# Kernel tuning notes

Measured on AMD Instinct MI355X. Metric: run time of the kernel, lower is better.

The kernel has to match this reference:

```python
import jax, jax.numpy as jnp
import numpy as np

B, N, IN_F, OUT_F = 32, 1024, 256, 256


def setup_inputs() -> dict:
    key = jax.random.key(0)
    k_adj, k_feat, k_w, k_b = jax.random.split(key, 4)
    adjacency = jax.random.uniform(k_adj, (B, N, N), dtype=jnp.float32)  # [B,N,N]
    features = jax.random.normal(k_feat, (B, N, IN_F), dtype=jnp.float32)  # [B,N,in]
    # 'thomas' init ~ uniform(-1/sqrt(fan_in), 1/sqrt(fan_in)) style; scale is
    # irrelevant to correctness-checking, use scaled normal.
    weight = jax.random.normal(k_w, (IN_F, OUT_F), dtype=jnp.float32) / np.sqrt(IN_F)
    bias = jax.random.normal(k_b, (OUT_F,), dtype=jnp.float32) / np.sqrt(IN_F)
    return {"adjacency": adjacency, "features": features, "weight": weight, "bias": bias}


def reference(adjacency, features, weight, bias) -> jnp.ndarray:
    # support = features @ weight : [B,N,out]
    support = jnp.einsum("bni,io->bno", features, weight)
    # output = bmm(adjacency, support) : [B,N,out]
    output = jnp.einsum("bnm,bmo->bno", adjacency, support)
    return output + bias
```

## Files before the change

### kernel.cpp

```cpp
#include <hip/hip_runtime.h>
#include <hip/hip_bf16.h>


typedef __attribute__((__ext_vector_type__(4))) float  f32x4;
typedef __attribute__((__ext_vector_type__(8))) __bf16 bf16x8;
typedef __attribute__((__ext_vector_type__(4))) __bf16 bf16x4;

#define BK 64

__device__ __forceinline__ void gld16(const void* g, void* l) {
  __builtin_amdgcn_global_load_lds(
      (const __attribute__((address_space(1))) unsigned int*)g,
      (__attribute__((address_space(3))) unsigned int*)l, 16, 0, 0);
}

__global__ __launch_bounds__(256) void k_wt(const float* __restrict__ w,
                                            __bf16* __restrict__ Wt) {
  __shared__ __bf16 T[64][65];
  const int bi = blockIdx.x >> 2;
  const int bj = blockIdx.x & 3;
  const int t  = threadIdx.x;
  const int r  = t >> 2;
  const int q  = t & 3;
  const float* src = w + (size_t)(bi * 64 + r) * 256 + bj * 64 + q * 16;
#pragma unroll
  for (int u = 0; u < 4; ++u) {
    f32x4 v = *(const f32x4*)(src + u * 4);
    T[r][q * 16 + u * 4 + 0] = (__bf16)v[0];
    T[r][q * 16 + u * 4 + 1] = (__bf16)v[1];
    T[r][q * 16 + u * 4 + 2] = (__bf16)v[2];
    T[r][q * 16 + u * 4 + 3] = (__bf16)v[3];
  }
  __syncthreads();
  bf16x8 h0, h1;
#pragma unroll
  for (int u = 0; u < 8; ++u) {
    h0[u] = T[q * 16 + u][r];
    h1[u] = T[q * 16 + 8 + u][r];
  }
  __bf16* d0 = Wt + ((size_t)(bi * 8 + q * 2) * 256 + (bj * 64 + r)) * 8;
  *(bf16x8*)d0          = h0;
  *(bf16x8*)(d0 + 2048) = h1;
}

template <int KTOT, int LDA, bool EPI_ST>
__global__ __launch_bounds__(512, 2) void k_gemm(
    const float* __restrict__ Aall, const __bf16* __restrict__ Bg_all,
    const float* __restrict__ bias, float* __restrict__ Out,
    __bf16* __restrict__ St) {
  __shared__ __bf16 Af[2][128 * 64];
  __shared__ __bf16 Bf[2][8 * 256 * 8];

  const int tid  = threadIdx.x;
  const int lane = tid & 63;
  const int wid  = tid >> 6;
  const int wr   = wid >> 2;
  const int wc   = wid & 3;
  const int l16  = lane & 15;
  const int g    = lane >> 4;

  int b, mblk;
  const float*  Ablk;
  const __bf16* Bblk;
  if constexpr (EPI_ST) {
    const int bx = blockIdx.x;
    b    = bx >> 3;
    mblk = bx & 7;
    Ablk = Aall + (size_t)bx * 128 * LDA;
    Bblk = Bg_all;
  } else {
    const int h  = blockIdx.x;
    const int lg = (h & 7) * 32 + (h >> 3);
    b    = lg >> 3;
    mblk = lg & 7;
    Ablk = Aall + (size_t)b * 1024 * 1024 + (size_t)mblk * 128 * LDA;
    Bblk = Bg_all + (size_t)b * 262144;
  }

  const int    srow = tid >> 2;
  const int    sq   = tid & 3;
  const float* asrc = Ablk + (size_t)srow * LDA + sq * 16;
  const int wof0 = srow * 64 + (((sq * 2)     ^ (srow & 7)) << 3);
  const int wof1 = srow * 64 + (((sq * 2 + 1) ^ (srow & 7)) << 3);

  const __bf16* bS[4];
#pragma unroll
  for (int i = 0; i < 4; ++i) bS[i] = Bblk + (size_t)(i * 512 + tid) * 8;

#define LOADA(S, k0)                                                          \
  {                                                                           \
    _Pragma("unroll") for (int u = 0; u < 4; ++u)                             \
        S[u] = *(const f32x4*)(asrc + (k0) + u * 4);                          \
  }
#define ISSUEB(buf, k0)                                                       \
  {                                                                           \
    const size_t koff = (size_t)((k0) >> 3) * 2048;                           \
    _Pragma("unroll") for (int i = 0; i < 4; ++i)                             \
        gld16(bS[i] + koff, &Bf[buf][(i * 512 + wid * 64) * 8]);              \
  }
#define CVTW(S, buf)                                                          \
  {                                                                           \
    bf16x8 h0 = {(__bf16)S[0][0], (__bf16)S[0][1], (__bf16)S[0][2],           \
                 (__bf16)S[0][3], (__bf16)S[1][0], (__bf16)S[1][1],           \
                 (__bf16)S[1][2], (__bf16)S[1][3]};                           \
    bf16x8 h1 = {(__bf16)S[2][0], (__bf16)S[2][1], (__bf16)S[2][2],           \
                 (__bf16)S[2][3], (__bf16)S[3][0], (__bf16)S[3][1],           \
                 (__bf16)S[3][2], (__bf16)S[3][3]};                           \
    *(bf16x8*)&Af[buf][wof0] = h0;                                            \
    *(bf16x8*)&Af[buf][wof1] = h1;                                            \
  }

  f32x4 S0[4], S1[4];

  f32x4 acc[4][4];
#pragma unroll
  for (int m = 0; m < 4; ++m)
#pragma unroll
    for (int n = 0; n < 4; ++n) acc[m][n] = (f32x4){0.f, 0.f, 0.f, 0.f};

  auto compute = [&](int buf) {
#pragma unroll
    for (int ks = 0; ks < 2; ++ks) {
      bf16x8 af[4], bv[4];
#pragma unroll
      for (int m = 0; m < 4; ++m) {
        const int row  = wr * 64 + m * 16 + l16;
        const int slot = (ks * 4 + g) ^ (row & 7);
        af[m] = *(const bf16x8*)&Af[buf][row * 64 + slot * 8];
      }
#pragma unroll
      for (int n = 0; n < 4; ++n) {
        const int col = wc * 64 + n * 16 + l16;
        bv[n] = *(const bf16x8*)&Bf[buf][((ks * 4 + g) * 256 + col) * 8];
      }
      __builtin_amdgcn_s_setprio(1);
#pragma unroll
      for (int m = 0; m < 4; ++m)
#pragma unroll
        for (int n = 0; n < 4; ++n)
          acc[m][n] = __builtin_amdgcn_mfma_f32_16x16x32_bf16(af[m], bv[n], acc[m][n], 0, 0, 0);
      __builtin_amdgcn_s_setprio(0);
    }
  };

  constexpr int NT = KTOT / BK;
  LOADA(S0, 0);
  ISSUEB(0, 0);
  LOADA(S1, BK);
  CVTW(S0, 0);
  __syncthreads();

  for (int t = 0; t < NT - 2; t += 2) {
    LOADA(S0, (t + 2) * BK);
    ISSUEB(1, (t + 1) * BK);
    compute(0);
    CVTW(S1, 1);
    __syncthreads();
    LOADA(S1, (t + 3) * BK);
    ISSUEB(0, (t + 2) * BK);
    compute(1);
    CVTW(S0, 0);
    __syncthreads();
  }
  ISSUEB(1, (NT - 1) * BK);
  compute(0);
  CVTW(S1, 1);
  __syncthreads();
  compute(1);

#undef LOADA
#undef ISSUEB
#undef CVTW

  const int rg = g * 4;
  if constexpr (EPI_ST) {
    __bf16* Stb = St + (size_t)b * 262144;
    const int gm0 = mblk * 128 + wr * 64;
#pragma unroll
    for (int n = 0; n < 4; ++n) {
      const int col = wc * 64 + n * 16 + l16;
#pragma unroll
      for (int m = 0; m < 4; ++m) {
        const int gm = gm0 + m * 16 + rg;
        __bf16* dst = Stb + (size_t)(gm >> 3) * 2048 + (size_t)col * 8 + (gm & 7);
        bf16x4 hh = {(__bf16)acc[m][n][0], (__bf16)acc[m][n][1],
                     (__bf16)acc[m][n][2], (__bf16)acc[m][n][3]};
        *(bf16x4*)dst = hh;
      }
    }
  } else {
    float* ob = Out + ((size_t)b * 1024 + (size_t)mblk * 128 + wr * 64) * 256;
#pragma unroll
    for (int n = 0; n < 4; ++n) {
      const int col = wc * 64 + n * 16 + l16;
      const float bvs = bias[col];
#pragma unroll
      for (int m = 0; m < 4; ++m) {
        const int row = m * 16 + rg;
#pragma unroll
        for (int r2 = 0; r2 < 4; ++r2)
          ob[(size_t)(row + r2) * 256 + col] = acc[m][n][r2] + bvs;
      }
    }
  }
}

extern "C" void kernel_launch(void* const* d_in, const int* in_sizes, int n_in,
                              void* d_out, int out_size, void* d_ws, size_t ws_size,
                              hipStream_t stream) {
  const float* adj  = (const float*)d_in[0];
  const float* feat = (const float*)d_in[1];
  const float* w    = (const float*)d_in[2];
  const float* bias = (const float*)d_in[3];
  float* out = (float*)d_out;

  __bf16* Wt = (__bf16*)d_ws;
  __bf16* St = (__bf16*)((char*)d_ws + 131072);

  k_wt<<<16, 256, 0, stream>>>(w, Wt);
  k_gemm<256, 256, true><<<256, 512, 0, stream>>>(feat, Wt, nullptr, nullptr, St);
  k_gemm<1024, 1024, false><<<256, 512, 0, stream>>>(adj, St, bias, out, nullptr);
}
```

Baseline: 53.07 us.

## Retile GEMMs to 128x128 blocks with 32x32 MFMA and single-buffered A

Halves the block tile along N (128x128 per 256-thread block, 512 blocks) and switches from 16x16x32 to 32x32x16 bf16 MFMA with four 32x32 accumulators per wave. The A tile becomes single-buffered in LDS, with the fp32-to-bf16 convert and write done mid-iteration behind a custom barrier using explicit waitcnt, and B is double-buffered via direct global-to-LDS loads. The aim is more blocks for occupancy and lower LDS read pressure per MFMA. The trade-off is that each fp32 adjacency row block is now read twice (once per N half), which raises global traffic.

```diff
diff --git a/kernel.cpp b/kernel.cpp
--- a/kernel.cpp
+++ b/kernel.cpp
@@ -2,9 +2,10 @@
 #include <hip/hip_bf16.h>
 
 
-typedef __attribute__((__ext_vector_type__(4))) float  f32x4;
-typedef __attribute__((__ext_vector_type__(8))) __bf16 bf16x8;
-typedef __attribute__((__ext_vector_type__(4))) __bf16 bf16x4;
+typedef __attribute__((__ext_vector_type__(4)))  float  f32x4;
+typedef __attribute__((__ext_vector_type__(16))) float  f32x16;
+typedef __attribute__((__ext_vector_type__(8)))  __bf16 bf16x8;
+typedef __attribute__((__ext_vector_type__(4)))  __bf16 bf16x4;
 
 #define BK 64
 
@@ -44,164 +45,199 @@
 }
 
 template <int KTOT, int LDA, bool EPI_ST>
-__global__ __launch_bounds__(512, 2) void k_gemm(
+__global__ __launch_bounds__(256, 2) void k_gemm(
     const float* __restrict__ Aall, const __bf16* __restrict__ Bg_all,
     const float* __restrict__ bias, float* __restrict__ Out,
     __bf16* __restrict__ St) {
-  __shared__ __bf16 Af[2][128 * 64];
-  __shared__ __bf16 Bf[2][8 * 256 * 8];
+  __shared__ __bf16 Af[128 * 64];
+  __shared__ __bf16 Bf[2][8 * 128 * 8];
 
   const int tid  = threadIdx.x;
   const int lane = tid & 63;
   const int wid  = tid >> 6;
-  const int wr   = wid >> 2;
-  const int wc   = wid & 3;
-  const int l16  = lane & 15;
-  const int g    = lane >> 4;
-
-  int b, mblk;
+  const int wm   = (wid >> 1) * 64;
+  const int wn   = (wid & 1) * 64;
+  const int l31  = lane & 31;
+  const int hi   = lane >> 5;
+
+  int b, mblk, nh;
   const float*  Ablk;
   const __bf16* Bblk;
   if constexpr (EPI_ST) {
     const int bx = blockIdx.x;
-    b    = bx >> 3;
-    mblk = bx & 7;
-    Ablk = Aall + (size_t)bx * 128 * LDA;
+    const int mt_lin = bx >> 1;
+    nh   = bx & 1;
+    b    = mt_lin >> 3;
+    mblk = mt_lin & 7;
+    Ablk = Aall + (size_t)mt_lin * 128 * LDA;
     Bblk = Bg_all;
   } else {
     const int h  = blockIdx.x;
-    const int lg = (h & 7) * 32 + (h >> 3);
-    b    = lg >> 3;
-    mblk = lg & 7;
+    const int lg = (h & 7) * 64 + (h >> 3);
+    b    = lg >> 4;
+    mblk = (lg >> 1) & 7;
+    nh   = lg & 1;
     Ablk = Aall + (size_t)b * 1024 * 1024 + (size_t)mblk * 128 * LDA;
     Bblk = Bg_all + (size_t)b * 262144;
   }
-
-  const int    srow = tid >> 2;
-  const int    sq   = tid & 3;
-  const float* asrc = Ablk + (size_t)srow * LDA + sq * 16;
-  const int wof0 = srow * 64 + (((sq * 2)     ^ (srow & 7)) << 3);
-  const int wof1 = srow * 64 + (((sq * 2 + 1) ^ (srow & 7)) << 3);
+  const int nb0 = nh * 128;
+
+  const int    srow = tid >> 1;
+  const int    skq  = (tid & 1) * 32;
+  const float* asrc = Ablk + (size_t)srow * LDA + skq;
+  const int    sr7  = srow & 7;
 
   const __bf16* bS[4];
 #pragma unroll
-  for (int i = 0; i < 4; ++i) bS[i] = Bblk + (size_t)(i * 512 + tid) * 8;
-
-#define LOADA(S, k0)                                                          \
+  for (int i = 0; i < 4; ++i) {
+    const int lin = i * 256 + tid;
+    bS[i] = Bblk + (size_t)(lin >> 7) * 2048 + (size_t)(nb0 + (lin & 127)) * 8;
+  }
+
+  f32x4 S[8];
+
+#define LOADA(k0)                                                             \
   {                                                                           \
-    _Pragma("unroll") for (int u = 0; u < 4; ++u)                             \
+    _Pragma("unroll") for (int u = 0; u < 8; ++u)                             \
         S[u] = *(const f32x4*)(asrc + (k0) + u * 4);                          \
+  }
+#define CVTW()                                                                \
+  {                                                                           \
+    _Pragma("unroll") for (int u2 = 0; u2 < 4; ++u2) {                        \
+      bf16x8 h = {(__bf16)S[2*u2][0],   (__bf16)S[2*u2][1],                   \
+                  (__bf16)S[2*u2][2],   (__bf16)S[2*u2][3],                   \
+                  (__bf16)S[2*u2+1][0], (__bf16)S[2*u2+1][1],                 \
+                  (__bf16)S[2*u2+1][2], (__bf16)S[2*u2+1][3]};                \
+      const int slot = (((tid & 1) * 4 + u2) ^ sr7);                          \
+      *(bf16x8*)&Af[srow * 64 + slot * 8] = h;                                \
+    }                                                                         \
   }
 #define ISSUEB(buf, k0)                                                       \
   {                                                                           \
     const size_t koff = (size_t)((k0) >> 3) * 2048;                           \
     _Pragma("unroll") for (int i = 0; i < 4; ++i)                             \
-        gld16(bS[i] + koff, &Bf[buf][(i * 512 + wid * 64) * 8]);              \
-  }
-#define CVTW(S, buf)                                                          \
-  {                                                                           \
-    bf16x8 h0 = {(__bf16)S[0][0], (__bf16)S[0][1], (__bf16)S[0][2],           \
-                 (__bf16)S[0][3], (__bf16)S[1][0], (__bf16)S[1][1],           \
-                 (__bf16)S[1][2], (__bf16)S[1][3]};                           \
-    bf16x8 h1 = {(__bf16)S[2][0], (__bf16)S[2][1], (__bf16)S[2][2],           \
-                 (__bf16)S[2][3], (__bf16)S[3][0], (__bf16)S[3][1],           \
-                 (__bf16)S[3][2], (__bf16)S[3][3]};                           \
-    *(bf16x8*)&Af[buf][wof0] = h0;                                            \
-    *(bf16x8*)&Af[buf][wof1] = h1;                                            \
-  }
-
-  f32x4 S0[4], S1[4];
-
-  f32x4 acc[4][4];
-#pragma unroll
-  for (int m = 0; m < 4; ++m)
-#pragma unroll
-    for (int n = 0; n < 4; ++n) acc[m][n] = (f32x4){0.f, 0.f, 0.f, 0.f};
-
-  auto compute = [&](int buf) {
-#pragma unroll
-    for (int ks = 0; ks < 2; ++ks) {
-      bf16x8 af[4], bv[4];
-#pragma unroll
-      for (int m = 0; m < 4; ++m) {
-        const int row  = wr * 64 + m * 16 + l16;
-        const int slot = (ks * 4 + g) ^ (row & 7);
-        af[m] = *(const bf16x8*)&Af[buf][row * 64 + slot * 8];
-      }
-#pragma unroll
-      for (int n = 0; n < 4; ++n) {
-        const int col = wc * 64 + n * 16 + l16;
-        bv[n] = *(const bf16x8*)&Bf[buf][((ks * 4 + g) * 256 + col) * 8];
-      }
-      __builtin_amdgcn_s_setprio(1);
-#pragma unroll
-      for (int m = 0; m < 4; ++m)
-#pragma unroll
-        for (int n = 0; n < 4; ++n)
-          acc[m][n] = __builtin_amdgcn_mfma_f32_16x16x32_bf16(af[m], bv[n], acc[m][n], 0, 0, 0);
-      __builtin_amdgcn_s_setprio(0);
+        gld16(bS[i] + koff, &Bf[buf][(i * 256 + wid * 64) * 8]);              \
+    asm volatile("" ::: "memory");                                            \
+  }
+#define MIDBAR asm volatile("s_waitcnt lgkmcnt(0)\n\ts_barrier" ::: "memory")
+#define SYNC8  asm volatile("s_waitcnt vmcnt(8) lgkmcnt(0)\n\ts_barrier" ::: "memory")
+#define SYNC0  asm volatile("s_waitcnt vmcnt(0) lgkmcnt(0)\n\ts_barrier" ::: "memory")
+
+  f32x16 acc[2][2];
+#pragma unroll
+  for (int mi = 0; mi < 2; ++mi)
+#pragma unroll
+    for (int ni = 0; ni < 2; ++ni)
+#pragma unroll
+      for (int r = 0; r < 16; ++r) acc[mi][ni][r] = 0.f;
+
+  auto dsread = [&](int p, int ks, bf16x8* af, bf16x8* bv) {
+#pragma unroll
+    for (int mi = 0; mi < 2; ++mi) {
+      const int row  = wm + mi * 32 + l31;
+      const int slot = (ks * 2 + hi) ^ (row & 7);
+      af[mi] = *(const bf16x8*)&Af[row * 64 + slot * 8];
+    }
+#pragma unroll
+    for (int ni = 0; ni < 2; ++ni) {
+      const int colx = wn + ni * 32 + l31;
+      bv[ni] = *(const bf16x8*)&Bf[p][((ks * 2 + hi) * 128 + colx) * 8];
     }
   };
+  auto domfma = [&](const bf16x8* af, const bf16x8* bv) {
+    __builtin_amdgcn_s_setprio(1);
+#pragma unroll
+    for (int mi = 0; mi < 2; ++mi)
+#pragma unroll
+      for (int ni = 0; ni < 2; ++ni)
+        acc[mi][ni] = __builtin_amdgcn_mfma_f32_32x32x16_bf16(af[mi], bv[ni], acc[mi][ni], 0, 0, 0);
+    __builtin_amdgcn_s_setprio(0);
+  };
 
   constexpr int NT = KTOT / BK;
-  LOADA(S0, 0);
+  LOADA(0);
   ISSUEB(0, 0);
-  LOADA(S1, BK);
-  CVTW(S0, 0);
-  __syncthreads();
-
-  for (int t = 0; t < NT - 2; t += 2) {
-    LOADA(S0, (t + 2) * BK);
-    ISSUEB(1, (t + 1) * BK);
-    compute(0);
-    CVTW(S1, 1);
-    __syncthreads();
-    LOADA(S1, (t + 3) * BK);
-    ISSUEB(0, (t + 2) * BK);
-    compute(1);
-    CVTW(S0, 0);
-    __syncthreads();
-  }
-  ISSUEB(1, (NT - 1) * BK);
-  compute(0);
-  CVTW(S1, 1);
-  __syncthreads();
-  compute(1);
+  CVTW();
+  LOADA(BK);
+  SYNC8;
+
+  for (int t = 0; t < NT - 2; ++t) {
+    const int p = t & 1;
+    ISSUEB(p ^ 1, (t + 1) * BK);
+    bf16x8 af[2], bv[2];
+    dsread(p, 0, af, bv); domfma(af, bv);
+    dsread(p, 1, af, bv); domfma(af, bv);
+    dsread(p, 2, af, bv); domfma(af, bv);
+    dsread(p, 3, af, bv);
+    MIDBAR;
+    CVTW();
+    LOADA((t + 2) * BK);
+    domfma(af, bv);
+    SYNC8;
+  }
+  {
+    ISSUEB(1, (NT - 1) * BK);
+    bf16x8 af[2], bv[2];
+    dsread(0, 0, af, bv); domfma(af, bv);
+    dsread(0, 1, af, bv); domfma(af, bv);
+    dsread(0, 2, af, bv); domfma(af, bv);
+    dsread(0, 3, af, bv);
+    MIDBAR;
+    CVTW();
+    domfma(af, bv);
+    SYNC0;
+  }
+  {
+    bf16x8 af[2], bv[2];
+    dsread(1, 0, af, bv); domfma(af, bv);
+    dsread(1, 1, af, bv); domfma(af, bv);
+    dsread(1, 2, af, bv); domfma(af, bv);
+    dsread(1, 3, af, bv); domfma(af, bv);
+  }
 
 #undef LOADA
+#undef CVTW
 #undef ISSUEB
-#undef CVTW
-
-  const int rg = g * 4;
+#undef MIDBAR
+#undef SYNC8
+#undef SYNC0
+
   if constexpr (EPI_ST) {
     __bf16* Stb = St + (size_t)b * 262144;
-    const int gm0 = mblk * 128 + wr * 64;
-#pragma unroll
-    for (int n = 0; n < 4; ++n) {
-      const int col = wc * 64 + n * 16 + l16;
-#pragma unroll
-      for (int m = 0; m < 4; ++m) {
-        const int gm = gm0 + m * 16 + rg;
-        __bf16* dst = Stb + (size_t)(gm >> 3) * 2048 + (size_t)col * 8 + (gm & 7);
-        bf16x4 hh = {(__bf16)acc[m][n][0], (__bf16)acc[m][n][1],
-                     (__bf16)acc[m][n][2], (__bf16)acc[m][n][3]};
-        *(bf16x4*)dst = hh;
+    const int gmbase = mblk * 128 + wm;
+#pragma unroll
+    for (int mi = 0; mi < 2; ++mi) {
+      const int base3 = ((gmbase + mi * 32) >> 3);
+#pragma unroll
+      for (int ni = 0; ni < 2; ++ni) {
+        const int col = nb0 + wn + ni * 32 + l31;
+#pragma unroll
+        for (int rq = 0; rq < 4; ++rq) {
+          bf16x4 hh = {(__bf16)acc[mi][ni][rq * 4 + 0],
+                       (__bf16)acc[mi][ni][rq * 4 + 1],
+                       (__bf16)acc[mi][ni][rq * 4 + 2],
+                       (__bf16)acc[mi][ni][rq * 4 + 3]};
+          __bf16* dst = Stb + (size_t)(base3 + rq) * 2048 + (size_t)col * 8 + 4 * hi;
+          *(bf16x4*)dst = hh;
+        }
       }
     }
   } else {
-    float* ob = Out + ((size_t)b * 1024 + (size_t)mblk * 128 + wr * 64) * 256;
-#pragma unroll
-    for (int n = 0; n < 4; ++n) {
-      const int col = wc * 64 + n * 16 + l16;
-      const float bvs = bias[col];
-#pragma unroll
-      for (int m = 0; m < 4; ++m) {
-        const int row = m * 16 + rg;
-#pragma unroll
-        for (int r2 = 0; r2 < 4; ++r2)
-          ob[(size_t)(row + r2) * 256 + col] = acc[m][n][r2] + bvs;
+    float* ob = Out + ((size_t)b * 1024 + (size_t)mblk * 128 + wm) * 256;
+#pragma unroll
+    for (int mi = 0; mi < 2; ++mi)
+#pragma unroll
+      for (int ni = 0; ni < 2; ++ni) {
+        const int col = nb0 + wn + ni * 32 + l31;
+        const float bvs = bias[col];
+#pragma unroll
+        for (int rq = 0; rq < 4; ++rq)
+#pragma unroll
+          for (int j = 0; j < 4; ++j) {
+            const int row = mi * 32 + rq * 8 + 4 * hi + j;
+            ob[(size_t)row * 256 + col] = acc[mi][ni][rq * 4 + j] + bvs;
+          }
       }
-    }
   }
 }
 
@@ -218,6 +254,6 @@
   __bf16* St = (__bf16*)((char*)d_ws + 131072);
 
   k_wt<<<16, 256, 0, stream>>>(w, Wt);
-  k_gemm<256, 256, true><<<256, 512, 0, stream>>>(feat, Wt, nullptr, nullptr, St);
-  k_gemm<1024, 1024, false><<<256, 512, 0, stream>>>(adj, St, bias, out, nullptr);
-}
+  k_gemm<256, 256, true><<<512, 256, 0, stream>>>(feat, Wt, nullptr, nullptr, St);
+  k_gemm<1024, 1024, false><<<512, 256, 0, stream>>>(adj, St, bias, out, nullptr);
+}
```

Measured after the change: 75.76 us. +42.8%, slower.

## Split main loop into half-tile phases with explicit barriers and vmcnt gating

Applied to the files above, without the earlier changes.

Restructures the GEMM main loop so each 64-wide K tile is processed in two half-steps: LDS fragment reads, issue of the next global loads, then a barrier and a block of 16 MFMAs. Full __syncthreads are replaced with raw s_barrier plus hand-written s_waitcnt (vmcnt(4)/lgkmcnt(0)) and sched_barrier. The aim is to interleave global loads, LDS writes and MFMA bursts more tightly and to avoid the conservative full waits that __syncthreads inserts. It relies on hand-counted outstanding-load numbers being correct, and the extra barriers could add stalls or introduce races if the counts are wrong.

```diff
diff --git a/kernel.cpp b/kernel.cpp
--- a/kernel.cpp
+++ b/kernel.cpp
@@ -97,6 +97,7 @@
     const size_t koff = (size_t)((k0) >> 3) * 2048;                           \
     _Pragma("unroll") for (int i = 0; i < 4; ++i)                             \
         gld16(bS[i] + koff, &Bf[buf][(i * 512 + wid * 64) * 8]);              \
+    asm volatile("" ::: "memory");                                            \
   }
 #define CVTW(S, buf)                                                          \
   {                                                                           \
@@ -109,6 +110,15 @@
     *(bf16x8*)&Af[buf][wof0] = h0;                                            \
     *(bf16x8*)&Af[buf][wof1] = h1;                                            \
   }
+#define BARIN                                                                 \
+  do {                                                                        \
+    __builtin_amdgcn_s_barrier();                                             \
+    asm volatile("s_waitcnt lgkmcnt(0)" ::: "memory");                        \
+    __builtin_amdgcn_sched_barrier(0);                                        \
+  } while (0)
+#define BAROUT __builtin_amdgcn_s_barrier()
+#define GATE4  asm volatile("s_waitcnt vmcnt(4)" ::: "memory")
+#define GATE0  asm volatile("s_waitcnt vmcnt(0)" ::: "memory")
 
   f32x4 S0[4], S1[4];
 
@@ -118,59 +128,79 @@
 #pragma unroll
     for (int n = 0; n < 4; ++n) acc[m][n] = (f32x4){0.f, 0.f, 0.f, 0.f};
 
-  auto compute = [&](int buf) {
-#pragma unroll
-    for (int ks = 0; ks < 2; ++ks) {
-      bf16x8 af[4], bv[4];
-#pragma unroll
-      for (int m = 0; m < 4; ++m) {
-        const int row  = wr * 64 + m * 16 + l16;
-        const int slot = (ks * 4 + g) ^ (row & 7);
-        af[m] = *(const bf16x8*)&Af[buf][row * 64 + slot * 8];
-      }
-#pragma unroll
-      for (int n = 0; n < 4; ++n) {
-        const int col = wc * 64 + n * 16 + l16;
-        bv[n] = *(const bf16x8*)&Bf[buf][((ks * 4 + g) * 256 + col) * 8];
-      }
-      __builtin_amdgcn_s_setprio(1);
-#pragma unroll
-      for (int m = 0; m < 4; ++m)
-#pragma unroll
-        for (int n = 0; n < 4; ++n)
-          acc[m][n] = __builtin_amdgcn_mfma_f32_16x16x32_bf16(af[m], bv[n], acc[m][n], 0, 0, 0);
-      __builtin_amdgcn_s_setprio(0);
+  auto dsread = [&](int p, int ks, bf16x8* af, bf16x8* bv) {
+#pragma unroll
+    for (int m = 0; m < 4; ++m) {
+      const int row  = wr * 64 + m * 16 + l16;
+      const int slot = (ks * 4 + g) ^ (row & 7);
+      af[m] = *(const bf16x8*)&Af[p][row * 64 + slot * 8];
+    }
+#pragma unroll
+    for (int n = 0; n < 4; ++n) {
+      const int col = wc * 64 + n * 16 + l16;
+      bv[n] = *(const bf16x8*)&Bf[p][((ks * 4 + g) * 256 + col) * 8];
     }
   };
+  auto mfma16 = [&](const bf16x8* af, const bf16x8* bv) {
+    __builtin_amdgcn_s_setprio(1);
+#pragma unroll
+    for (int m = 0; m < 4; ++m)
+#pragma unroll
+      for (int n = 0; n < 4; ++n)
+        acc[m][n] = __builtin_amdgcn_mfma_f32_16x16x32_bf16(af[m], bv[n], acc[m][n], 0, 0, 0);
+    __builtin_amdgcn_s_setprio(0);
+  };
 
   constexpr int NT = KTOT / BK;
+  bf16x8 af[4], bv[4];
+
   LOADA(S0, 0);
   ISSUEB(0, 0);
   LOADA(S1, BK);
   CVTW(S0, 0);
-  __syncthreads();
+  asm volatile("s_waitcnt vmcnt(4) lgkmcnt(0)" ::: "memory");
+  __builtin_amdgcn_s_barrier();
 
   for (int t = 0; t < NT - 2; t += 2) {
+    dsread(0, 0, af, bv);
+    ISSUEB(1, (t + 1) * BK);
+    BARIN;  mfma16(af, bv);  BAROUT;
+    dsread(0, 1, af, bv);
+    CVTW(S1, 1);
     LOADA(S0, (t + 2) * BK);
-    ISSUEB(1, (t + 1) * BK);
-    compute(0);
-    CVTW(S1, 1);
-    __syncthreads();
+    BARIN;  mfma16(af, bv);
+    GATE4;
+    BAROUT;
+    dsread(1, 0, af, bv);
+    ISSUEB(0, (t + 2) * BK);
+    BARIN;  mfma16(af, bv);  BAROUT;
+    dsread(1, 1, af, bv);
+    CVTW(S0, 0);
     LOADA(S1, (t + 3) * BK);
-    ISSUEB(0, (t + 2) * BK);
-    compute(1);
-    CVTW(S0, 0);
-    __syncthreads();
-  }
+    BARIN;  mfma16(af, bv);
+    GATE4;
+    BAROUT;
+  }
+  dsread(0, 0, af, bv);
   ISSUEB(1, (NT - 1) * BK);
-  compute(0);
+  BARIN;  mfma16(af, bv);  BAROUT;
+  dsread(0, 1, af, bv);
   CVTW(S1, 1);
-  __syncthreads();
-  compute(1);
+  BARIN;  mfma16(af, bv);
+  GATE0;
+  BAROUT;
+  dsread(1, 0, af, bv);
+  mfma16(af, bv);
+  dsread(1, 1, af, bv);
+  mfma16(af, bv);
 
 #undef LOADA
 #undef ISSUEB
 #undef CVTW
+#undef BARIN
+#undef BAROUT
+#undef GATE4
+#undef GATE0
 
   const int rg = g * 4;
   if constexpr (EPI_ST) {
```

Measured after the change: 54.79 us. +3.3%, slower.

## Shrink GEMM tiles to 64x256, halve BK, and use explicit vmcnt-gated pipeline

Applied to the files above, without the earlier changes.

Each GEMM block now covers a 64-row by 256-column tile with 256 threads and BK=32. This doubles the grid to 512 blocks with up to 4 blocks per CU, for better occupancy and wave coverage. The A tile now uses a padded LDS stride instead of an XOR swizzle. The pipeline prefetches both B buffers, and __syncthreads is replaced by inline s_waitcnt vmcnt/barrier gates so that loads stay in flight across iterations. Output stores become nontemporal. The cost is that each block reuses B from LDS across half as many rows, so each block does more global traffic per FLOP, and the hand-counted vmcnt values are fragile.

```diff
diff --git a/kernel.cpp b/kernel.cpp
--- a/kernel.cpp
+++ b/kernel.cpp
@@ -6,7 +6,8 @@
 typedef __attribute__((__ext_vector_type__(8))) __bf16 bf16x8;
 typedef __attribute__((__ext_vector_type__(4))) __bf16 bf16x4;
 
-#define BK 64
+#define BK 32
+#define LDPA 40
 
 __device__ __forceinline__ void gld16(const void* g, void* l) {
   __builtin_amdgcn_global_load_lds(
@@ -44,73 +45,68 @@
 }
 
 template <int KTOT, int LDA, bool EPI_ST>
-__global__ __launch_bounds__(512, 2) void k_gemm(
+__global__ __launch_bounds__(256, 4) void k_gemm(
     const float* __restrict__ Aall, const __bf16* __restrict__ Bg_all,
     const float* __restrict__ bias, float* __restrict__ Out,
     __bf16* __restrict__ St) {
-  __shared__ __bf16 Af[2][128 * 64];
-  __shared__ __bf16 Bf[2][8 * 256 * 8];
+  __shared__ __bf16 Af[2][64 * LDPA];
+  __shared__ __bf16 Bf[2][4 * 256 * 8];
 
   const int tid  = threadIdx.x;
   const int lane = tid & 63;
   const int wid  = tid >> 6;
-  const int wr   = wid >> 2;
-  const int wc   = wid & 3;
+  const int wc   = wid;
   const int l16  = lane & 15;
   const int g    = lane >> 4;
 
   int b, mblk;
   const float*  Ablk;
   const __bf16* Bblk;
+  const int h  = blockIdx.x;
+  const int lg = (h & 7) * 64 + (h >> 3);
+  b    = lg >> 4;
+  mblk = lg & 15;
   if constexpr (EPI_ST) {
-    const int bx = blockIdx.x;
-    b    = bx >> 3;
-    mblk = bx & 7;
-    Ablk = Aall + (size_t)bx * 128 * LDA;
+    Ablk = Aall + (size_t)lg * 64 * LDA;
     Bblk = Bg_all;
   } else {
-    const int h  = blockIdx.x;
-    const int lg = (h & 7) * 32 + (h >> 3);
-    b    = lg >> 3;
-    mblk = lg & 7;
-    Ablk = Aall + (size_t)b * 1024 * 1024 + (size_t)mblk * 128 * LDA;
+    Ablk = Aall + (size_t)b * 1024 * 1024 + (size_t)mblk * 64 * LDA;
     Bblk = Bg_all + (size_t)b * 262144;
   }
 
   const int    srow = tid >> 2;
   const int    sq   = tid & 3;
-  const float* asrc = Ablk + (size_t)srow * LDA + sq * 16;
-  const int wof0 = srow * 64 + (((sq * 2)     ^ (srow & 7)) << 3);
-  const int wof1 = srow * 64 + (((sq * 2 + 1) ^ (srow & 7)) << 3);
+  const float* asrc = Ablk + (size_t)srow * LDA + sq * 8;
+  const int    wof  = srow * LDPA + sq * 8;
 
   const __bf16* bS[4];
 #pragma unroll
-  for (int i = 0; i < 4; ++i) bS[i] = Bblk + (size_t)(i * 512 + tid) * 8;
+  for (int i = 0; i < 4; ++i) bS[i] = Bblk + (size_t)(i * 256 + tid) * 8;
 
 #define LOADA(S, k0)                                                          \
   {                                                                           \
-    _Pragma("unroll") for (int u = 0; u < 4; ++u)                             \
-        S[u] = *(const f32x4*)(asrc + (k0) + u * 4);                          \
+    S[0] = *(const f32x4*)(asrc + (k0));                                      \
+    S[1] = *(const f32x4*)(asrc + (k0) + 4);                                  \
   }
 #define ISSUEB(buf, k0)                                                       \
   {                                                                           \
     const size_t koff = (size_t)((k0) >> 3) * 2048;                           \
     _Pragma("unroll") for (int i = 0; i < 4; ++i)                             \
-        gld16(bS[i] + koff, &Bf[buf][(i * 512 + wid * 64) * 8]);              \
+        gld16(bS[i] + koff, &Bf[buf][(i * 256 + wid * 64) * 8]);              \
+    asm volatile("" ::: "memory");                                            \
   }
 #define CVTW(S, buf)                                                          \
   {                                                                           \
-    bf16x8 h0 = {(__bf16)S[0][0], (__bf16)S[0][1], (__bf16)S[0][2],           \
+    bf16x8 hh = {(__bf16)S[0][0], (__bf16)S[0][1], (__bf16)S[0][2],           \
                  (__bf16)S[0][3], (__bf16)S[1][0], (__bf16)S[1][1],           \
                  (__bf16)S[1][2], (__bf16)S[1][3]};                           \
-    bf16x8 h1 = {(__bf16)S[2][0], (__bf16)S[2][1], (__bf16)S[2][2],           \
-                 (__bf16)S[2][3], (__bf16)S[3][0], (__bf16)S[3][1],           \
-                 (__bf16)S[3][2], (__bf16)S[3][3]};                           \
-    *(bf16x8*)&Af[buf][wof0] = h0;                                            \
-    *(bf16x8*)&Af[buf][wof1] = h1;                                            \
-  }
-
-  f32x4 S0[4], S1[4];
+    *(bf16x8*)&Af[buf][wof] = hh;                                             \
+  }
+#define GATE2 asm volatile("s_waitcnt vmcnt(2) lgkmcnt(0)\n\ts_barrier" ::: "memory")
+#define GATE6 asm volatile("s_waitcnt vmcnt(6) lgkmcnt(0)\n\ts_barrier" ::: "memory")
+#define GATE0 asm volatile("s_waitcnt vmcnt(0) lgkmcnt(0)\n\ts_barrier" ::: "memory")
+
+  f32x4 S0[2], S1[2];
 
   f32x4 acc[4][4];
 #pragma unroll
@@ -118,64 +114,64 @@
 #pragma unroll
     for (int n = 0; n < 4; ++n) acc[m][n] = (f32x4){0.f, 0.f, 0.f, 0.f};
 
-  auto compute = [&](int buf) {
-#pragma unroll
-    for (int ks = 0; ks < 2; ++ks) {
-      bf16x8 af[4], bv[4];
-#pragma unroll
-      for (int m = 0; m < 4; ++m) {
-        const int row  = wr * 64 + m * 16 + l16;
-        const int slot = (ks * 4 + g) ^ (row & 7);
-        af[m] = *(const bf16x8*)&Af[buf][row * 64 + slot * 8];
-      }
-#pragma unroll
-      for (int n = 0; n < 4; ++n) {
-        const int col = wc * 64 + n * 16 + l16;
-        bv[n] = *(const bf16x8*)&Bf[buf][((ks * 4 + g) * 256 + col) * 8];
-      }
-      __builtin_amdgcn_s_setprio(1);
-#pragma unroll
-      for (int m = 0; m < 4; ++m)
-#pragma unroll
-        for (int n = 0; n < 4; ++n)
-          acc[m][n] = __builtin_amdgcn_mfma_f32_16x16x32_bf16(af[m], bv[n], acc[m][n], 0, 0, 0);
-      __builtin_amdgcn_s_setprio(0);
-    }
+  auto compute = [&](int p) {
+    bf16x8 af[4], bv[4];
+#pragma unroll
+    for (int m = 0; m < 4; ++m) {
+      const int row = m * 16 + l16;
+      af[m] = *(const bf16x8*)&Af[p][row * LDPA + g * 8];
+    }
+#pragma unroll
+    for (int n = 0; n < 4; ++n) {
+      const int col = wc * 64 + n * 16 + l16;
+      bv[n] = *(const bf16x8*)&Bf[p][(g * 256 + col) * 8];
+    }
+    __builtin_amdgcn_s_setprio(1);
+#pragma unroll
+    for (int m = 0; m < 4; ++m)
+#pragma unroll
+      for (int n = 0; n < 4; ++n)
+        acc[m][n] = __builtin_amdgcn_mfma_f32_16x16x32_bf16(af[m], bv[n], acc[m][n], 0, 0, 0);
+    __builtin_amdgcn_s_setprio(0);
   };
 
   constexpr int NT = KTOT / BK;
   LOADA(S0, 0);
   ISSUEB(0, 0);
   LOADA(S1, BK);
+  ISSUEB(1, BK);
   CVTW(S0, 0);
-  __syncthreads();
+  GATE6;
 
   for (int t = 0; t < NT - 2; t += 2) {
-    LOADA(S0, (t + 2) * BK);
-    ISSUEB(1, (t + 1) * BK);
     compute(0);
     CVTW(S1, 1);
-    __syncthreads();
-    LOADA(S1, (t + 3) * BK);
+    LOADA(S0, (t + 2) * BK);
+    GATE2;
     ISSUEB(0, (t + 2) * BK);
+
     compute(1);
     CVTW(S0, 0);
-    __syncthreads();
-  }
-  ISSUEB(1, (NT - 1) * BK);
+    LOADA(S1, (t + 3) * BK);
+    GATE2;
+    ISSUEB(1, (t + 3) * BK);
+  }
   compute(0);
   CVTW(S1, 1);
-  __syncthreads();
+  GATE0;
   compute(1);
 
 #undef LOADA
 #undef ISSUEB
 #undef CVTW
+#undef GATE2
+#undef GATE6
+#undef GATE0
 
   const int rg = g * 4;
   if constexpr (EPI_ST) {
     __bf16* Stb = St + (size_t)b * 262144;
-    const int gm0 = mblk * 128 + wr * 64;
+    const int gm0 = mblk * 64;
 #pragma unroll
     for (int n = 0; n < 4; ++n) {
       const int col = wc * 64 + n * 16 + l16;
@@ -189,7 +185,7 @@
       }
     }
   } else {
-    float* ob = Out + ((size_t)b * 1024 + (size_t)mblk * 128 + wr * 64) * 256;
+    float* ob = Out + ((size_t)b * 1024 + (size_t)mblk * 64) * 256;
 #pragma unroll
     for (int n = 0; n < 4; ++n) {
       const int col = wc * 64 + n * 16 + l16;
@@ -199,7 +195,8 @@
         const int row = m * 16 + rg;
 #pragma unroll
         for (int r2 = 0; r2 < 4; ++r2)
-          ob[(size_t)(row + r2) * 256 + col] = acc[m][n][r2] + bvs;
+          __builtin_nontemporal_store(acc[m][n][r2] + bvs,
+                                      &ob[(size_t)(row + r2) * 256 + col]);
       }
     }
   }
@@ -218,6 +215,6 @@
   __bf16* St = (__bf16*)((char*)d_ws + 131072);
 
   k_wt<<<16, 256, 0, stream>>>(w, Wt);
-  k_gemm<256, 256, true><<<256, 512, 0, stream>>>(feat, Wt, nullptr, nullptr, St);
-  k_gemm<1024, 1024, false><<<256, 512, 0, stream>>>(adj, St, bias, out, nullptr);
-}
+  k_gemm<256, 256, true><<<512, 256, 0, stream>>>(feat, Wt, nullptr, nullptr, St);
+  k_gemm<1024, 1024, false><<<512, 256, 0, stream>>>(adj, St, bias, out, nullptr);
+}
```

After: 53.61 us. Within noise of the previous version (+1.0%).
